# Kernel tuning notes

Measured on AMD Instinct MI355X. Metric: run time of the kernel, lower is better.

Reference implementation:

```python
import jax, jax.numpy as jnp
import numpy as np

COMMITMENT_COST = 0.25
B, T, D = 32, 2048, 64
K = 1024


def setup_inputs() -> dict:
    key = jax.random.key(0)
    k1, k2 = jax.random.split(key)
    inputs = jax.random.normal(k1, (B, T, D), dtype=jnp.float32)
    # codebook init: uniform(-1/K, 1/K) in the original; use same scale
    embedding = jax.random.uniform(k2, (K, D), dtype=jnp.float32,
                                   minval=-1.0 / K, maxval=1.0 / K)
    return {"inputs": inputs, "embedding": embedding}


def reference(inputs, embedding):
    Bb, Tt, Dd = inputs.shape
    flat = inputs.reshape(-1, Dd)  # [N, D]
    dist = (jnp.sum(flat * flat, axis=1, keepdims=True)
            + jnp.sum(embedding * embedding, axis=1)[None, :]
            - 2.0 * (flat @ embedding.T))
    encoding_indices = jnp.argmin(dist, axis=1)  # [N]
    quantized = embedding[encoding_indices].reshape(Bb, Tt, Dd)
    # commitment loss: mse(stop_grad(quantized), inputs)
    e_latent_loss = jnp.mean((jax.lax.stop_gradient(quantized) - inputs) ** 2)
    vq_loss = COMMITMENT_COST * e_latent_loss
    codebook_loss = jnp.zeros((), dtype=jnp.float32)
    # straight-through estimator
    quantized_st = inputs + jax.lax.stop_gradient(quantized - inputs)
    return (quantized_st, encoding_indices.reshape(Bb, Tt),
            vq_loss, e_latent_loss, codebook_loss)
```

## Files before the change

### kernel.cpp

```cpp
#include <hip/hip_runtime.h>
#include <hip/hip_bf16.h>
#include <math.h>


typedef __attribute__((ext_vector_type(8))) short bf16x8;
typedef __attribute__((ext_vector_type(4))) float f32x4;

namespace {
constexpr int NROWS  = 65536;
constexpr int DDIM   = 64;
constexpr int KCODES = 1024;
constexpr float EPSB = 4e-5f;

constexpr size_t WS_LOSS = 0;
constexpr size_t WS_CNT  = 64;
constexpr size_t WS_SE   = 256;
constexpr size_t WS_EHB  = 8192;
constexpr size_t WS_ELB  = WS_EHB + (size_t)65536 * 2;
constexpr size_t WS_BIDX = WS_ELB + (size_t)65536 * 2;
constexpr size_t WS_LIST = WS_BIDX + (size_t)NROWS * 4;
constexpr size_t WS_KEY  = WS_LIST + (size_t)NROWS * 4;
constexpr size_t WS_MV   = WS_KEY + (size_t)NROWS * 8;
constexpr size_t WS_KV   = WS_MV + (size_t)2 * NROWS * 8;
}

__device__ inline short f2bf(float v) {
  __hip_bfloat16 h = __float2bfloat16(v);
  return *reinterpret_cast<short*>(&h);
}
__device__ inline float bf2f(short s) {
  __hip_bfloat16 h;
  *reinterpret_cast<short*>(&h) = s;
  return __bfloat162float(h);
}
__device__ inline f32x4 mfma16(bf16x8 a, bf16x8 b, f32x4 c) {
  return __builtin_amdgcn_mfma_f32_16x16x32_bf16(a, b, c, 0, 0, 0);
}
__device__ inline unsigned int fflip(unsigned int b) {
  return b ^ ((unsigned int)((int)b >> 31) | 0x80000000u);
}

__global__ __launch_bounds__(256) void vq_prep(const float* __restrict__ emb,
                                               float* __restrict__ se,
                                               short* __restrict__ ehB,
                                               short* __restrict__ elB,
                                               unsigned long long* __restrict__ keyBest,
                                               double* __restrict__ loss_accum,
                                               int* __restrict__ cnt) {
  #pragma clang fp contract(off)
  const int gid = blockIdx.x * 256 + (int)threadIdx.x;
  if (gid == 0) { *loss_accum = 0.0; *cnt = 0; }
  keyBest[gid] = ~0ull;

  if (gid < KCODES) {
    const float* e = emb + (size_t)gid * DDIM;
    float r[8];
    #pragma unroll
    for (int j = 0; j < 8; ++j) r[j] = e[j] * e[j];
    #pragma unroll
    for (int i = 8; i < DDIM; i += 8) {
      #pragma unroll
      for (int j = 0; j < 8; ++j) r[j] += e[i + j] * e[i + j];
    }
    se[gid] = ((r[0] + r[1]) + (r[2] + r[3])) + ((r[4] + r[5]) + (r[6] + r[7]));
  }

  if (gid < 8192) {
    const int t  = gid >> 7;
    const int dc = (gid >> 6) & 1;
    const int l  = gid & 63;
    const int code = t * 16 + (l & 15);
    const int d0   = dc * 32 + (l >> 4) * 8;
    const float* ep = emb + (size_t)code * DDIM + d0;
    const size_t ob = ((size_t)(t * 2 + dc) * 64 + l) * 8;
    #pragma unroll
    for (int i = 0; i < 8; ++i) {
      const float v = ep[i];
      const short h = f2bf(v);
      ehB[ob + i] = h;
      elB[ob + i] = f2bf(v - bf2f(h));
    }
  }
}

__global__ __launch_bounds__(256, 2) void vq_fused(const float* __restrict__ x,
                                                   const short* __restrict__ ehB,
                                                   const short* __restrict__ elB,
                                                   const float* __restrict__ se,
                                                   float2* __restrict__ mv,
                                                   unsigned long long* __restrict__ kv) {
  #pragma clang fp contract(off)
  __shared__ float sel[KCODES];
  const int tid  = (int)threadIdx.x;
  const int l    = tid & 63;
  const int wid  = tid >> 6;
  const int half = (int)blockIdx.x & 1;
  const int rblk = (int)blockIdx.x >> 1;
  #pragma unroll
  for (int i = 0; i < 4; ++i) sel[i * 256 + tid] = se[i * 256 + tid];
  __syncthreads();

  const int wrb = rblk * 128 + wid * 32;
  bf16x8 xh[2][2], xl[2][2];
  #pragma unroll
  for (int rt = 0; rt < 2; ++rt) {
    const float* xp = x + (size_t)(wrb + rt * 16 + (l & 15)) * DDIM + (l >> 4) * 8;
    #pragma unroll
    for (int dc = 0; dc < 2; ++dc) {
      const float4 v0 = *reinterpret_cast<const float4*>(xp + dc * 32);
      const float4 v1 = *reinterpret_cast<const float4*>(xp + dc * 32 + 4);
      const float vv[8] = {v0.x, v0.y, v0.z, v0.w, v1.x, v1.y, v1.z, v1.w};
      #pragma unroll
      for (int i = 0; i < 8; ++i) {
        const short h = f2bf(vv[i]);
        xh[rt][dc][i] = h;
        xl[rt][dc][i] = f2bf(vv[i] - bf2f(h));
      }
    }
  }

  float m1v[2][4], m2v[2][4];
  int   m1t[2][4];
  #pragma unroll
  for (int rt = 0; rt < 2; ++rt)
    #pragma unroll
    for (int r = 0; r < 4; ++r) { m1v[rt][r] = INFINITY; m2v[rt][r] = INFINITY; m1t[rt][r] = 0; }

  const size_t lb = (size_t)l * 8;
  const int t0 = half * 32;
#define FRAGLD(buf, tt, half2) \
  (*reinterpret_cast<const bf16x8*>((buf) + (size_t)(tt) * 1024 + (half2) * 512 + lb))

  bf16x8 c0 = FRAGLD(ehB, t0, 0), c1 = FRAGLD(ehB, t0, 1),
         c2 = FRAGLD(elB, t0, 0), c3 = FRAGLD(elB, t0, 1);
  bf16x8 n0 = FRAGLD(ehB, t0 + 1, 0), n1 = FRAGLD(ehB, t0 + 1, 1),
         n2 = FRAGLD(elB, t0 + 1, 0), n3 = FRAGLD(elB, t0 + 1, 1);

  const f32x4 kz = {0.f, 0.f, 0.f, 0.f};
  #pragma unroll 4
  for (int tt = 0; tt < 32; ++tt) {
    const int t = t0 + tt;
    const int tf = (tt + 2 < 32) ? t + 2 : t0 + 31;
    bf16x8 f0 = FRAGLD(ehB, tf, 0), f1 = FRAGLD(ehB, tf, 1),
           f2 = FRAGLD(elB, tf, 0), f3 = FRAGLD(elB, tf, 1);

    f32x4 a0, a1;
    a0 = mfma16(xh[0][0], c0, kz);  a1 = mfma16(xh[1][0], c0, kz);
    a0 = mfma16(xh[0][1], c1, a0);  a1 = mfma16(xh[1][1], c1, a1);
    a0 = mfma16(xh[0][0], c2, a0);  a1 = mfma16(xh[1][0], c2, a1);
    a0 = mfma16(xh[0][1], c3, a0);  a1 = mfma16(xh[1][1], c3, a1);
    a0 = mfma16(xl[0][0], c0, a0);  a1 = mfma16(xl[1][0], c0, a1);
    a0 = mfma16(xl[0][1], c1, a0);  a1 = mfma16(xl[1][1], c1, a1);

    const float sev = sel[t * 16 + (l & 15)];
    #pragma unroll
    for (int r = 0; r < 4; ++r) {
      {
        const float d = __builtin_fmaf(-2.0f, a0[r], sev);
        const bool c = d < m1v[0][r];
        m2v[0][r] = fminf(m2v[0][r], fmaxf(m1v[0][r], d));
        m1t[0][r] = c ? t : m1t[0][r];
        m1v[0][r] = fminf(m1v[0][r], d);
      }
      {
        const float d = __builtin_fmaf(-2.0f, a1[r], sev);
        const bool c = d < m1v[1][r];
        m2v[1][r] = fminf(m2v[1][r], fmaxf(m1v[1][r], d));
        m1t[1][r] = c ? t : m1t[1][r];
        m1v[1][r] = fminf(m1v[1][r], d);
      }
    }
    c0 = n0; c1 = n1; c2 = n2; c3 = n3;
    n0 = f0; n1 = f1; n2 = f2; n3 = f3;
  }
#undef FRAGLD

  const int colbase = l & 15;
  #pragma unroll
  for (int rt = 0; rt < 2; ++rt) {
    #pragma unroll
    for (int r = 0; r < 4; ++r) {
      float m1 = m1v[rt][r], m2 = m2v[rt][r];
      unsigned long long key =
          ((unsigned long long)fflip(__float_as_uint(m1)) << 32)
          | (unsigned)(m1t[rt][r] * 16 + colbase);
      #pragma unroll
      for (int off = 1; off < 16; off <<= 1) {
        const unsigned long long ok = __shfl_xor(key, off, 16);
        const float om1 = __shfl_xor(m1, off, 16);
        const float om2 = __shfl_xor(m2, off, 16);
        m2 = fminf(fminf(m2, om2), fmaxf(m1, om1));
        m1 = fminf(m1, om1);
        key = (ok < key) ? ok : key;
      }
      if (colbase == 0) {
        const int row = wrb + rt * 16 + (l >> 4) * 4 + r;
        mv[(size_t)half * NROWS + row] = make_float2(m1, m2);
        kv[(size_t)half * NROWS + row] = key;
      }
    }
  }
}

__global__ __launch_bounds__(256) void vq_combine(const float2* __restrict__ mv,
                                                  const unsigned long long* __restrict__ kv,
                                                  int* __restrict__ bidx,
                                                  int* __restrict__ list,
                                                  int* __restrict__ cnt) {
  const int gid = blockIdx.x * 256 + (int)threadIdx.x;
  const int l = (int)threadIdx.x & 63;
  const float2 a = mv[gid];
  const float2 b = mv[(size_t)NROWS + gid];
  const unsigned long long ka = kv[gid];
  const unsigned long long kb = kv[(size_t)NROWS + gid];
  const float m1g = fminf(a.x, b.x);
  const float m2g = fminf(fminf(a.y, b.y), fmaxf(a.x, b.x));
  const unsigned long long kg = (ka < kb) ? ka : kb;
  const bool cert = m2g > m1g + EPSB;
  bidx[gid] = cert ? (int)(kg & 0xffffffffull) : -1;

  const unsigned long long mask = __ballot(!cert);
  int base = 0;
  if (l == 0 && mask) base = atomicAdd(cnt, (int)__popcll(mask));
  base = __shfl(base, 0, 64);
  if (!cert) {
    const int off = (int)__popcll(mask & ((1ull << l) - 1ull));
    list[base + off] = gid;
  }
}

__global__ __launch_bounds__(256) void vq_exact(const float* __restrict__ x,
                                                const float* __restrict__ emb,
                                                const float* __restrict__ se,
                                                const int* __restrict__ list,
                                                const int* __restrict__ cnt,
                                                unsigned long long* __restrict__ keyBest) {
  #pragma clang fp contract(off)
  __shared__ __align__(16) float eL[64 * DDIM];
  const int part = (int)blockIdx.x & 15;
  const int j0 = part * 64;

  {
    const float4* src = reinterpret_cast<const float4*>(emb + (size_t)j0 * DDIM);
    float4* dst = reinterpret_cast<float4*>(eL);
    #pragma unroll
    for (int i = 0; i < 4; ++i)
      dst[i * 256 + (int)threadIdx.x] = src[i * 256 + (int)threadIdx.x];
  }
  __syncthreads();

  const int n = *cnt;
  const int l  = (int)threadIdx.x & 63;
  const int wv = (int)threadIdx.x >> 6;

  for (int rb = (int)blockIdx.x >> 4; rb * 256 < n; rb += 32) {
    const int idx = rb * 256 + wv * 64 + l;
    const bool act = idx < n;
    const int row = act ? list[idx] : 0;
    const float4* xr4 = reinterpret_cast<const float4*>(x + (size_t)row * DDIM);

    float xv[DDIM];
    #pragma unroll
    for (int q = 0; q < 16; ++q) {
      const float4 v = xr4[q];
      xv[q * 4 + 0] = v.x; xv[q * 4 + 1] = v.y;
      xv[q * 4 + 2] = v.z; xv[q * 4 + 3] = v.w;
    }

    float rr[8];
    #pragma unroll
    for (int j = 0; j < 8; ++j) rr[j] = xv[j] * xv[j];
    #pragma unroll
    for (int i = 8; i < DDIM; i += 8) {
      #pragma unroll
      for (int j = 0; j < 8; ++j) rr[j] += xv[i + j] * xv[i + j];
    }
    const float sx = ((rr[0] + rr[1]) + (rr[2] + rr[3])) + ((rr[4] + rr[5]) + (rr[6] + rr[7]));

    unsigned long long best = ~0ull;
    #pragma unroll 1
    for (int g = 0; g < 16; ++g) {
      const int jb = g * 4;
      const float4* e0 = reinterpret_cast<const float4*>(eL + (jb + 0) * DDIM);
      const float4* e1 = reinterpret_cast<const float4*>(eL + (jb + 1) * DDIM);
      const float4* e2 = reinterpret_cast<const float4*>(eL + (jb + 2) * DDIM);
      const float4* e3 = reinterpret_cast<const float4*>(eL + (jb + 3) * DDIM);
      float a0 = 0.f, a1 = 0.f, a2 = 0.f, a3 = 0.f;
      #pragma unroll
      for (int q = 0; q < 16; ++q) {
        const float4 v0 = e0[q], v1 = e1[q], v2 = e2[q], v3 = e3[q];
        const float xa = xv[q * 4 + 0], xb = xv[q * 4 + 1];
        const float xc = xv[q * 4 + 2], xd = xv[q * 4 + 3];
        a0 = __builtin_fmaf(xa, v0.x, a0); a0 = __builtin_fmaf(xb, v0.y, a0);
        a0 = __builtin_fmaf(xc, v0.z, a0); a0 = __builtin_fmaf(xd, v0.w, a0);
        a1 = __builtin_fmaf(xa, v1.x, a1); a1 = __builtin_fmaf(xb, v1.y, a1);
        a1 = __builtin_fmaf(xc, v1.z, a1); a1 = __builtin_fmaf(xd, v1.w, a1);
        a2 = __builtin_fmaf(xa, v2.x, a2); a2 = __builtin_fmaf(xb, v2.y, a2);
        a2 = __builtin_fmaf(xc, v2.z, a2); a2 = __builtin_fmaf(xd, v2.w, a2);
        a3 = __builtin_fmaf(xa, v3.x, a3); a3 = __builtin_fmaf(xb, v3.y, a3);
        a3 = __builtin_fmaf(xc, v3.z, a3); a3 = __builtin_fmaf(xd, v3.w, a3);
      }
      const int j = j0 + jb;
      const float T0 = sx + se[j + 0];
      const float T1 = sx + se[j + 1];
      const float T2 = sx + se[j + 2];
      const float T3 = sx + se[j + 3];
      const float di0 = __builtin_fmaf(-2.0f, a0, T0);
      const float di1 = __builtin_fmaf(-2.0f, a1, T1);
      const float di2 = __builtin_fmaf(-2.0f, a2, T2);
      const float di3 = __builtin_fmaf(-2.0f, a3, T3);
      unsigned long long k;
      k = ((unsigned long long)fflip(__float_as_uint(di0)) << 32) | (unsigned)(j + 0);
      best = (k < best) ? k : best;
      k = ((unsigned long long)fflip(__float_as_uint(di1)) << 32) | (unsigned)(j + 1);
      best = (k < best) ? k : best;
      k = ((unsigned long long)fflip(__float_as_uint(di2)) << 32) | (unsigned)(j + 2);
      best = (k < best) ? k : best;
      k = ((unsigned long long)fflip(__float_as_uint(di3)) << 32) | (unsigned)(j + 3);
      best = (k < best) ? k : best;
    }
    if (act) atomicMin(&keyBest[row], best);
  }
}

__global__ __launch_bounds__(256) void vq_finalize(const float* __restrict__ x,
                                                   const float* __restrict__ emb,
                                                   const int* __restrict__ bidx,
                                                   const unsigned long long* __restrict__ keyBest,
                                                   float* __restrict__ out,
                                                   double* __restrict__ loss_accum) {
  #pragma clang fp contract(off)
  __shared__ float wsum[4];
  const int tid = (int)threadIdx.x;
  const int l   = tid & 63;
  const int wid = tid >> 6;
  const int sub = l >> 4;
  const int q16 = l & 15;
  float lacc = 0.f;

  #pragma unroll
  for (int it = 0; it < 4; ++it) {
    const int row = blockIdx.x * 64 + it * 16 + wid * 4 + sub;
    int bi = bidx[row];
    if (bi < 0) bi = (int)(keyBest[row] & 0xffffffffull);
    const float4 xv = reinterpret_cast<const float4*>(x)[(size_t)row * 16 + q16];
    const float4 ev = reinterpret_cast<const float4*>(emb)[(size_t)bi * 16 + q16];
    const float da = ev.x - xv.x;
    const float db = ev.y - xv.y;
    const float dc = ev.z - xv.z;
    const float dd = ev.w - xv.w;
    float4 o;
    o.x = xv.x + da; o.y = xv.y + db; o.z = xv.z + dc; o.w = xv.w + dd;
    reinterpret_cast<float4*>(out)[(size_t)row * 16 + q16] = o;
    lacc += da * da + db * db + dc * dc + dd * dd;
    if (q16 == 0) out[(size_t)NROWS * DDIM + row] = (float)bi;
  }
  #pragma unroll
  for (int off = 32; off > 0; off >>= 1) lacc += __shfl_down(lacc, off, 64);
  if (l == 0) wsum[wid] = lacc;
  __syncthreads();
  if (tid == 0)
    atomicAdd(loss_accum, (double)(wsum[0] + wsum[1] + wsum[2] + wsum[3]));
}

__global__ void vq_scalars(const double* __restrict__ loss_accum,
                           float* __restrict__ out) {
  if (threadIdx.x == 0 && blockIdx.x == 0) {
    const double mm = *loss_accum / (double)((size_t)NROWS * DDIM);
    const float el = (float)mm;
    float* tail = out + (size_t)NROWS * DDIM + NROWS;
    tail[0] = 0.25f * el;
    tail[1] = el;
    tail[2] = 0.0f;
  }
}

extern "C" void kernel_launch(void* const* d_in, const int* in_sizes, int n_in,
                              void* d_out, int out_size, void* d_ws, size_t ws_size,
                              hipStream_t stream) {
  const float* x   = (const float*)d_in[0];
  const float* emb = (const float*)d_in[1];
  float* out = (float*)d_out;
  char* ws = (char*)d_ws;

  double* loss_accum = (double*)(ws + WS_LOSS);
  int*    cnt        = (int*)(ws + WS_CNT);
  float*  se         = (float*)(ws + WS_SE);
  short*  ehB        = (short*)(ws + WS_EHB);
  short*  elB        = (short*)(ws + WS_ELB);
  int*    bidx       = (int*)(ws + WS_BIDX);
  int*    list       = (int*)(ws + WS_LIST);
  unsigned long long* keyBest = (unsigned long long*)(ws + WS_KEY);
  float2* mv         = (float2*)(ws + WS_MV);
  unsigned long long* kv = (unsigned long long*)(ws + WS_KV);

  vq_prep<<<NROWS / 256, 256, 0, stream>>>(emb, se, ehB, elB, keyBest,
                                           loss_accum, cnt);
  vq_fused<<<(NROWS / 128) * 2, 256, 0, stream>>>(x, ehB, elB, se, mv, kv);
  vq_combine<<<NROWS / 256, 256, 0, stream>>>(mv, kv, bidx, list, cnt);
  vq_exact<<<512, 256, 0, stream>>>(x, emb, se, list, cnt, keyBest);
  vq_finalize<<<NROWS / 64, 256, 0, stream>>>(x, emb, bidx, keyBest, out,
                                              loss_accum);
  vq_scalars<<<1, 64, 0, stream>>>(loss_accum, out);
}
```

Before: 112.1 us.

## Split codebook scan into quarters and rebalance exact-fallback kernel work distribution

The fused MFMA distance kernel now splits the codebook into four quarters instead of two. That doubles the grid and halves per-block work and shared memory, and the combine kernel merges four partial top-2 results. The exact fp32 fallback kernel changes to 64-thread blocks that loop over (row-block, 32-code part) tasks sized to the actual ambiguous-row count, rather than a fixed 512×256 layout. The goal is better occupancy and load balance. In exchange it adds more partial-result memory traffic and extra combine work, and the fallback reloads the codebook tile into shared memory for each task.

```diff
diff --git a/kernel.cpp b/kernel.cpp
--- a/kernel.cpp
+++ b/kernel.cpp
@@ -21,7 +21,7 @@
 constexpr size_t WS_LIST = WS_BIDX + (size_t)NROWS * 4;
 constexpr size_t WS_KEY  = WS_LIST + (size_t)NROWS * 4;
 constexpr size_t WS_MV   = WS_KEY + (size_t)NROWS * 8;
-constexpr size_t WS_KV   = WS_MV + (size_t)2 * NROWS * 8;
+constexpr size_t WS_KV   = WS_MV + (size_t)4 * NROWS * 8;
 }
 
 __device__ inline short f2bf(float v) {
@@ -90,14 +90,14 @@
                                                    float2* __restrict__ mv,
                                                    unsigned long long* __restrict__ kv) {
   #pragma clang fp contract(off)
-  __shared__ float sel[KCODES];
+  __shared__ float sel[256];
   const int tid  = (int)threadIdx.x;
   const int l    = tid & 63;
   const int wid  = tid >> 6;
-  const int half = (int)blockIdx.x & 1;
-  const int rblk = (int)blockIdx.x >> 1;
-  #pragma unroll
-  for (int i = 0; i < 4; ++i) sel[i * 256 + tid] = se[i * 256 + tid];
+  const int quar = (int)blockIdx.x & 3;
+  const int rblk = (int)blockIdx.x >> 2;
+  const int t0   = quar * 16;
+  sel[tid] = se[t0 * 16 + tid];
   __syncthreads();
 
   const int wrb = rblk * 128 + wid * 32;
@@ -127,7 +127,6 @@
     for (int r = 0; r < 4; ++r) { m1v[rt][r] = INFINITY; m2v[rt][r] = INFINITY; m1t[rt][r] = 0; }
 
   const size_t lb = (size_t)l * 8;
-  const int t0 = half * 32;
 #define FRAGLD(buf, tt, half2) \
   (*reinterpret_cast<const bf16x8*>((buf) + (size_t)(tt) * 1024 + (half2) * 512 + lb))
 
@@ -138,9 +137,9 @@
 
   const f32x4 kz = {0.f, 0.f, 0.f, 0.f};
   #pragma unroll 4
-  for (int tt = 0; tt < 32; ++tt) {
+  for (int tt = 0; tt < 16; ++tt) {
     const int t = t0 + tt;
-    const int tf = (tt + 2 < 32) ? t + 2 : t0 + 31;
+    const int tf = (tt + 2 < 16) ? t + 2 : t0 + 15;
     bf16x8 f0 = FRAGLD(ehB, tf, 0), f1 = FRAGLD(ehB, tf, 1),
            f2 = FRAGLD(elB, tf, 0), f3 = FRAGLD(elB, tf, 1);
 
@@ -152,7 +151,7 @@
     a0 = mfma16(xl[0][0], c0, a0);  a1 = mfma16(xl[1][0], c0, a1);
     a0 = mfma16(xl[0][1], c1, a0);  a1 = mfma16(xl[1][1], c1, a1);
 
-    const float sev = sel[t * 16 + (l & 15)];
+    const float sev = sel[tt * 16 + (l & 15)];
     #pragma unroll
     for (int r = 0; r < 4; ++r) {
       {
@@ -195,8 +194,8 @@
       }
       if (colbase == 0) {
         const int row = wrb + rt * 16 + (l >> 4) * 4 + r;
-        mv[(size_t)half * NROWS + row] = make_float2(m1, m2);
-        kv[(size_t)half * NROWS + row] = key;
+        mv[(size_t)quar * NROWS + row] = make_float2(m1, m2);
+        kv[(size_t)quar * NROWS + row] = key;
       }
     }
   }
@@ -209,13 +208,21 @@
                                                   int* __restrict__ cnt) {
   const int gid = blockIdx.x * 256 + (int)threadIdx.x;
   const int l = (int)threadIdx.x & 63;
-  const float2 a = mv[gid];
-  const float2 b = mv[(size_t)NROWS + gid];
-  const unsigned long long ka = kv[gid];
-  const unsigned long long kb = kv[(size_t)NROWS + gid];
-  const float m1g = fminf(a.x, b.x);
-  const float m2g = fminf(fminf(a.y, b.y), fmaxf(a.x, b.x));
-  const unsigned long long kg = (ka < kb) ? ka : kb;
+  const float2 A = mv[gid];
+  const float2 B = mv[(size_t)NROWS + gid];
+  const float2 C = mv[(size_t)2 * NROWS + gid];
+  const float2 D = mv[(size_t)3 * NROWS + gid];
+  unsigned long long kg = kv[gid];
+  {
+    unsigned long long k2 = kv[(size_t)NROWS + gid];     kg = (k2 < kg) ? k2 : kg;
+    k2 = kv[(size_t)2 * NROWS + gid];                    kg = (k2 < kg) ? k2 : kg;
+    k2 = kv[(size_t)3 * NROWS + gid];                    kg = (k2 < kg) ? k2 : kg;
+  }
+  const float lo1 = fminf(A.x, B.x), hi1 = fmaxf(A.x, B.x);
+  const float lo2 = fminf(C.x, D.x), hi2 = fmaxf(C.x, D.x);
+  const float m1g = fminf(lo1, lo2);
+  const float sec = fminf(fmaxf(lo1, lo2), fminf(hi1, hi2));
+  const float m2g = fminf(sec, fminf(fminf(A.y, B.y), fminf(C.y, D.y)));
   const bool cert = m2g > m1g + EPSB;
   bidx[gid] = cert ? (int)(kg & 0xffffffffull) : -1;
 
@@ -229,32 +236,34 @@
   }
 }
 
-__global__ __launch_bounds__(256) void vq_exact(const float* __restrict__ x,
-                                                const float* __restrict__ emb,
-                                                const float* __restrict__ se,
-                                                const int* __restrict__ list,
-                                                const int* __restrict__ cnt,
-                                                unsigned long long* __restrict__ keyBest) {
+__global__ __launch_bounds__(64) void vq_exact(const float* __restrict__ x,
+                                               const float* __restrict__ emb,
+                                               const float* __restrict__ se,
+                                               const int* __restrict__ list,
+                                               const int* __restrict__ cnt,
+                                               unsigned long long* __restrict__ keyBest) {
   #pragma clang fp contract(off)
-  __shared__ __align__(16) float eL[64 * DDIM];
-  const int part = (int)blockIdx.x & 15;
-  const int j0 = part * 64;
-
-  {
-    const float4* src = reinterpret_cast<const float4*>(emb + (size_t)j0 * DDIM);
-    float4* dst = reinterpret_cast<float4*>(eL);
-    #pragma unroll
-    for (int i = 0; i < 4; ++i)
-      dst[i * 256 + (int)threadIdx.x] = src[i * 256 + (int)threadIdx.x];
-  }
-  __syncthreads();
-
+  __shared__ __align__(16) float eL[32 * DDIM];
   const int n = *cnt;
-  const int l  = (int)threadIdx.x & 63;
-  const int wv = (int)threadIdx.x >> 6;
-
-  for (int rb = (int)blockIdx.x >> 4; rb * 256 < n; rb += 32) {
-    const int idx = rb * 256 + wv * 64 + l;
+  if (n == 0) return;
+  const int nrb = (n + 63) >> 6;
+  const int ntasks = nrb * 32;
+  const int l = (int)threadIdx.x;
+
+  for (int t = (int)blockIdx.x; t < ntasks; t += (int)gridDim.x) {
+    const int part = t & 31;
+    const int rb   = t >> 5;
+    const int j0   = part * 32;
+
+    {
+      const float4* src = reinterpret_cast<const float4*>(emb + (size_t)j0 * DDIM);
+      float4* dst = reinterpret_cast<float4*>(eL);
+      #pragma unroll
+      for (int i = 0; i < 8; ++i) dst[i * 64 + l] = src[i * 64 + l];
+    }
+    __syncthreads();
+
+    const int idx = rb * 64 + l;
     const bool act = idx < n;
     const int row = act ? list[idx] : 0;
     const float4* xr4 = reinterpret_cast<const float4*>(x + (size_t)row * DDIM);
@@ -279,7 +288,7 @@
 
     unsigned long long best = ~0ull;
     #pragma unroll 1
-    for (int g = 0; g < 16; ++g) {
+    for (int g = 0; g < 8; ++g) {
       const int jb = g * 4;
       const float4* e0 = reinterpret_cast<const float4*>(eL + (jb + 0) * DDIM);
       const float4* e1 = reinterpret_cast<const float4*>(eL + (jb + 1) * DDIM);
@@ -320,6 +329,7 @@
       best = (k < best) ? k : best;
     }
     if (act) atomicMin(&keyBest[row], best);
+    __syncthreads();
   }
 }
 
@@ -396,9 +406,9 @@
 
   vq_prep<<<NROWS / 256, 256, 0, stream>>>(emb, se, ehB, elB, keyBest,
                                            loss_accum, cnt);
-  vq_fused<<<(NROWS / 128) * 2, 256, 0, stream>>>(x, ehB, elB, se, mv, kv);
+  vq_fused<<<(NROWS / 128) * 4, 256, 0, stream>>>(x, ehB, elB, se, mv, kv);
   vq_combine<<<NROWS / 256, 256, 0, stream>>>(mv, kv, bidx, list, cnt);
-  vq_exact<<<512, 256, 0, stream>>>(x, emb, se, list, cnt, keyBest);
+  vq_exact<<<2048, 64, 0, stream>>>(x, emb, se, list, cnt, keyBest);
   vq_finalize<<<NROWS / 64, 256, 0, stream>>>(x, emb, bidx, keyBest, out,
                                               loss_accum);
   vq_scalars<<<1, 64, 0, stream>>>(loss_accum, out);
```

After: 98.73 us (median of 2 runs). 1.14x faster.
